# Kernel optimization log

Hardware: AMD Instinct MI355X
Metric: run time of the kernel (lower is better)

## Reference

```python
import jax, jax.numpy as jnp
import numpy as np

DIM = 1024
HEADS = 16
DIM_HEAD = 64
INNER = HEADS * DIM_HEAD
SCALE = DIM_HEAD ** -0.5


def setup_inputs() -> dict:
    key = jax.random.key(0)
    ks = jax.random.split(key, 9)
    B, N = 4, 4096
    x = jax.random.normal(ks[0], (B, N, DIM), dtype=jnp.float32)
    mask = jnp.ones((B, N), dtype=bool)
    s = 0.02
    W_qkv = jax.random.normal(ks[1], (DIM, INNER * 3), dtype=jnp.float32) * s
    w_q = jax.random.normal(ks[2], (DIM_HEAD,), dtype=jnp.float32) * s
    w_k = jax.random.normal(ks[3], (DIM_HEAD,), dtype=jnp.float32) * s
    W_r = jax.random.normal(ks[4], (DIM_HEAD, DIM_HEAD), dtype=jnp.float32) * s
    b_r = jnp.zeros((DIM_HEAD,), dtype=jnp.float32)
    W_out = jax.random.normal(ks[5], (INNER, DIM), dtype=jnp.float32) * s
    b_out = jnp.zeros((DIM,), dtype=jnp.float32)
    return {"x": x, "mask": mask, "W_qkv": W_qkv, "w_q": w_q, "w_k": w_k,
            "W_r": W_r, "b_r": b_r, "W_out": W_out, "b_out": b_out}


def reference(x, mask, W_qkv, w_q, w_k, W_r, b_r, W_out, b_out):
    B, N, D = x.shape
    h, dh = HEADS, DIM_HEAD
    mask_value = -jnp.finfo(x.dtype).max

    qkv = x @ W_qkv                                  # [B,N,3*inner]
    q, k, v = jnp.split(qkv, 3, axis=-1)
    tohead = lambda t: t.reshape(B, N, h, dh).transpose(0, 2, 1, 3)  # b h n d
    q, k, v = tohead(q), tohead(k), tohead(v)
    m = mask[:, None, :]                             # b 1 n

    # global query via softmax-pooled per-token logits
    q_logits = jnp.einsum('bhnd,d->bhn', q, w_q) * SCALE
    q_attn = jax.nn.softmax(jnp.where(m, q_logits, mask_value), axis=-1)
    global_q = jnp.einsum('bhn,bhnd->bhd', q_attn, q)[:, :, None, :]  # b h 1 d

    k = k * global_q
    k_logits = jnp.einsum('bhnd,d->bhn', k, w_k) * SCALE
    k_attn = jax.nn.softmax(jnp.where(m, k_logits, mask_value), axis=-1)
    global_k = jnp.einsum('bhn,bhnd->bhd', k_attn, k)[:, :, None, :]  # b h 1 d

    v = v * global_k
    r = jnp.einsum('bhnd,de->bhne', v, W_r) + b_r + q  # to_r(v) + q
    r = r.transpose(0, 2, 1, 3).reshape(B, N, h * dh)  # b n (h d)
    return r @ W_out + b_out
```

## Files before the change

### kernel.cpp

```cpp
#include <hip/hip_runtime.h>
#include <hip/hip_bf16.h>
#include <math.h>

#define B_    4
#define N_    4096
#define D_    1024
#define H_    16
#define DH_   64
#define M_TOT (B_ * N_)
#define QKV3  (3 * D_)
#define SCALE_ 0.125f
#define NSPLIT 8

typedef float f32x4 __attribute__((ext_vector_type(4)));
typedef __bf16 bf16x8 __attribute__((ext_vector_type(8)));
typedef unsigned short u16;
typedef unsigned int u32;

__device__ __forceinline__ float bf2f(u16 u) {
    union { u32 i; float f; } v; v.i = ((u32)u) << 16; return v.f;
}
__device__ __forceinline__ u16 f2bf(float f) {
    union { float f; u32 i; } v; v.f = f;
    u32 r = (v.i + 0x7fffu + ((v.i >> 16) & 1u)) >> 16;
    return (u16)r;
}

__global__ __launch_bounds__(256) void prep(const float* __restrict__ x, u16* __restrict__ xb,
                                            const float* __restrict__ Wqkv, u16* __restrict__ wqkv,
                                            const float* __restrict__ Wout, u16* __restrict__ wout) {
    __shared__ float t[32][33];
    const int bid = blockIdx.x, tid = threadIdx.x;
    if (bid < 16384) {
        const int i = bid * 256 + tid;
        float4 v = ((const float4*)x)[i];
        ushort4 o;
        o.x = f2bf(v.x); o.y = f2bf(v.y); o.z = f2bf(v.z); o.w = f2bf(v.w);
        ((ushort4*)xb)[i] = o;
        return;
    }
    const float* in; u16* out; int K, N, bx, by;
    if (bid < 16384 + 3072) {
        const int b2 = bid - 16384;
        in = Wqkv; out = wqkv; K = D_; N = QKV3; bx = b2 % 96; by = b2 / 96;
    } else {
        const int b2 = bid - 19456;
        in = Wout; out = wout; K = D_; N = D_; bx = b2 & 31; by = b2 >> 5;
    }
    const int n0 = bx * 32, k0 = by * 32;
    const int tx = tid & 31, ty = tid >> 5;
#pragma unroll
    for (int r = 0; r < 32; r += 8)
        t[ty + r][tx] = in[(size_t)(k0 + ty + r) * N + n0 + tx];
    __syncthreads();
#pragma unroll
    for (int r = 0; r < 32; r += 8)
        out[(size_t)(n0 + ty + r) * K + k0 + tx] = f2bf(t[tx][ty + r]);
}

#define BM 256
#define BN 256
#define BK 32

template <bool SCATTER, bool SWIZ>
__global__ __launch_bounds__(512, 2) void gemm_bt(const u16* __restrict__ A,
                                                  const u16* __restrict__ Bt,
                                                  void* __restrict__ Cout,
                                                  const float* __restrict__ bias,
                                                  int M, int N, int K) {
    __shared__ u16 lds[65536];
    const int tid = threadIdx.x;
    const int lane = tid & 63, wave = tid >> 6;
    const int wm = wave >> 2, wn = wave & 3;
    u32 bx = blockIdx.x, by = blockIdx.y;
    if (SWIZ) {
        const u32 nwg = gridDim.x * gridDim.y;
        const u32 lid = by * gridDim.x + bx;
        const u32 chunk = nwg >> 3;
        const u32 nid = (lid & 7) * chunk + (lid >> 3);
        bx = nid % gridDim.x; by = nid / gridDim.x;
    }
    const int m0 = by * BM, n0 = bx * BN;

    const int srow = tid >> 2;
    const int scol = 8 * ((tid & 3) ^ ((tid >> 3) & 3));
    const u16* aSrc = A + (size_t)(m0 + srow) * K + scol;
    const u16* bSrc = Bt + (size_t)(n0 + srow) * K + scol;
    const u32 dOff = (u32)wave * 512u;

    const int cbu = 8 * ((lane >> 4) ^ ((lane >> 1) & 3));
    const u32 arow = (u32)(wm * 128 + (lane & 15)) * 32u + cbu;
    const u32 brow = 32768u + (u32)(wn * 64 + (lane & 15)) * 32u + cbu;

    f32x4 acc[8][4] = {};

#define GLOAD(src, off) __builtin_amdgcn_global_load_lds(                          \
        (__attribute__((address_space(1))) const void*)(src),                      \
        (__attribute__((address_space(3))) void*)&lds[off], 16, 0, 0)
#define STAGE(t) { const size_t ko = (size_t)(t) * BK; const u32 sb_ = ((t) & 3) * 8192u; \
        GLOAD(aSrc + ko,                   sb_ + dOff);                            \
        GLOAD(aSrc + ko + (size_t)128 * K, sb_ + 4096u + dOff);                    \
        GLOAD(bSrc + ko,                   32768u + sb_ + dOff);                   \
        GLOAD(bSrc + ko + (size_t)128 * K, 32768u + sb_ + 4096u + dOff); }

    const int NT = K >> 5;
    STAGE(0); STAGE(1); STAGE(2);

    for (int t = 0; t < NT; ++t) {
        if (t + 3 <= NT)      asm volatile("s_waitcnt vmcnt(8)" ::: "memory");
        else if (t + 2 == NT) asm volatile("s_waitcnt vmcnt(4)" ::: "memory");
        else                  asm volatile("s_waitcnt vmcnt(0)" ::: "memory");
        __builtin_amdgcn_s_barrier();
        if (t + 3 < NT) STAGE(t + 3);

        const u32 sb = (u32)(t & 3) * 8192u;
        bf16x8 af[8], bfr[4];
#pragma unroll
        for (int i = 0; i < 8; i++) af[i] = *(const bf16x8*)&lds[sb + arow + i * 512];
#pragma unroll
        for (int j = 0; j < 4; j++) bfr[j] = *(const bf16x8*)&lds[sb + brow + j * 512];
        __builtin_amdgcn_s_setprio(1);
#pragma unroll
        for (int i = 0; i < 8; i++)
#pragma unroll
            for (int j = 0; j < 4; j++)
                acc[i][j] = __builtin_amdgcn_mfma_f32_16x16x32_bf16(af[i], bfr[j], acc[i][j], 0, 0, 0);
        __builtin_amdgcn_s_setprio(0);
    }
#undef STAGE
#undef GLOAD

    __syncthreads();
    const int cr = (lane >> 4) * 4;
    const int cc = lane & 15;
    u16* reg = &lds[(u32)wave * 8192u];

    if (SCATTER) {
#pragma unroll
        for (int i = 0; i < 8; i++)
#pragma unroll
            for (int j = 0; j < 4; j++)
#pragma unroll
                for (int r = 0; r < 4; r++)
                    reg[(i * 16 + cr + r) * 64 + j * 16 + cc] = f2bf(acc[i][j][r]);
        const int colb = n0 + wn * 64;
        const int part = colb >> 10, hh = (colb >> 6) & (H_ - 1);
        const int grow0 = m0 + wm * 128;
        const int bb = grow0 >> 12, nn0 = grow0 & (N_ - 1);
        u16* plane = (u16*)Cout + (((size_t)(part * B_ + bb) * H_ + hh) * N_) * DH_;
        const int lr8 = lane >> 3, le = (lane & 7) * 8;
#pragma unroll
        for (int p = 0; p < 16; p++) {
            const int lr = p * 8 + lr8;
            const uint4 w = *(const uint4*)&reg[lr * 64 + le];
            *(uint4*)(plane + (size_t)(nn0 + lr) * DH_ + le) = w;
        }
    } else {
        float* regf = (float*)reg;
        const int lr4 = lane >> 4, le4 = (lane & 15) * 4;
        float bv[4];
#pragma unroll
        for (int j = 0; j < 4; j++)
            bv[j] = bias ? bias[n0 + wn * 64 + j * 16 + cc] : 0.f;
#pragma unroll
        for (int h = 0; h < 2; h++) {
#pragma unroll
            for (int i2 = 0; i2 < 4; i2++) {
                const int i = h * 4 + i2;
#pragma unroll
                for (int j = 0; j < 4; j++)
#pragma unroll
                    for (int r = 0; r < 4; r++)
                        regf[(i2 * 16 + cr + r) * 64 + j * 16 + cc] = acc[i][j][r] + bv[j];
            }
#pragma unroll
            for (int p = 0; p < 16; p++) {
                const int lr = p * 4 + lr4;
                const float4 w = *(const float4*)&regf[lr * 64 + le4];
                *(float4*)((float*)Cout + (size_t)(m0 + wm * 128 + h * 64 + lr) * N
                           + n0 + wn * 64 + le4) = w;
            }
            if (!h) __syncthreads();
        }
    }
}

template <bool KPHASE>
__global__ __launch_bounds__(256) void pool_partial(const u16* __restrict__ plane,
                                                    const float* __restrict__ wvec,
                                                    const float* __restrict__ partq,
                                                    float* __restrict__ part) {
    __shared__ float sm[32], sl[32], sacc[32][64];
    __shared__ float gqsh[64];
    const int bh = blockIdx.x, s = blockIdx.y;
    const int tid = threadIdx.x;
    const int sub = tid >> 3, j = tid & 7;
    const size_t base = (size_t)bh * N_ * DH_ + (size_t)s * (N_ / NSPLIT) * DH_ + j * 8;

    if (KPHASE) {
        if (tid < 64) {
            float M = -INFINITY;
            for (int t = 0; t < NSPLIT; t++) M = fmaxf(M, partq[((size_t)bh * NSPLIT + t) * 66]);
            float L = 0.f, ssum = 0.f;
            for (int t = 0; t < NSPLIT; t++) {
                const float* o = partq + ((size_t)bh * NSPLIT + t) * 66;
                const float e = __expf(o[0] - M);
                L += o[1] * e;
                ssum += o[2 + tid] * e;
            }
            gqsh[tid] = ssum / L;
        }
        __syncthreads();
    }

    float wv[8], gq[8];
#pragma unroll
    for (int i = 0; i < 8; i++) wv[i] = wvec[j * 8 + i];
    if (KPHASE) {
#pragma unroll
        for (int i = 0; i < 8; i++) gq[i] = gqsh[j * 8 + i];
    }

    float m = -INFINITY, l = 0.f, acc[8];
#pragma unroll
    for (int i = 0; i < 8; i++) acc[i] = 0.f;
    const int ITER = N_ / NSPLIT / 32;
    uint4 raw = *(const uint4*)(plane + base + (size_t)sub * DH_);
    for (int it = 0; it < ITER; it++) {
        uint4 nxt;
        if (it + 1 < ITER)
            nxt = *(const uint4*)(plane + base + (size_t)((it + 1) * 32 + sub) * DH_);
        const u16* pu = (const u16*)&raw;
        float f[8], p = 0.f;
#pragma unroll
        for (int i = 0; i < 8; i++) {
            f[i] = bf2f(pu[i]);
            if (KPHASE) f[i] *= gq[i];
            p += f[i] * wv[i];
        }
        p += __shfl_xor(p, 1); p += __shfl_xor(p, 2); p += __shfl_xor(p, 4);
        p *= SCALE_;
        const float mn = fmaxf(m, p);
        const float sc = __expf(m - mn);
        const float w = __expf(p - mn);
        m = mn; l = l * sc + w;
#pragma unroll
        for (int i = 0; i < 8; i++) acc[i] = acc[i] * sc + w * f[i];
        raw = nxt;
    }
    if (j == 0) { sm[sub] = m; sl[sub] = l; }
#pragma unroll
    for (int i = 0; i < 8; i++) sacc[sub][j * 8 + i] = acc[i];
    __syncthreads();
    if (tid < 64) {
        float M = -INFINITY;
        for (int g = 0; g < 32; g++) M = fmaxf(M, sm[g]);
        float L = 0.f, ssum = 0.f;
        for (int g = 0; g < 32; g++) {
            const float e = __expf(sm[g] - M);
            L += sl[g] * e;
            ssum += sacc[g][tid] * e;
        }
        float* o = part + ((size_t)bh * NSPLIT + s) * 66;
        if (tid == 0) { o[0] = M; o[1] = L; }
        o[2 + tid] = ssum;
    }
}

__global__ __launch_bounds__(256) void apply_r_mfma(const u16* __restrict__ qkv,
                                                    const float* __restrict__ Wr,
                                                    const float* __restrict__ br,
                                                    const float* __restrict__ partk,
                                                    u16* __restrict__ rout) {
    __shared__ u16 Mt[64][136];
    __shared__ float gksh[64];
    __shared__ u16 rb[4][64 * 64];
    const int bh = blockIdx.y;
    const int b = bh >> 4, h = bh & 15;
    const int tid = threadIdx.x, lane = tid & 63, wave = tid >> 6;

    if (tid < 64) {
        float M = -INFINITY;
        for (int t = 0; t < NSPLIT; t++) M = fmaxf(M, partk[((size_t)bh * NSPLIT + t) * 66]);
        float L = 0.f, ssum = 0.f;
        for (int t = 0; t < NSPLIT; t++) {
            const float* o = partk + ((size_t)bh * NSPLIT + t) * 66;
            const float e = __expf(o[0] - M);
            L += o[1] * e;
            ssum += o[2 + tid] * e;
        }
        gksh[tid] = ssum / L;
    }
    __syncthreads();

    for (int idx = tid; idx < 4096; idx += 256) {
        const int d = idx >> 6, e = idx & 63;
        Mt[e][d] = f2bf(gksh[d] * Wr[idx]);
        Mt[e][64 + d] = (d == e) ? (u16)0x3F80 : (u16)0;
    }
    __syncthreads();

    const size_t qbase = (size_t)bh * N_ * DH_;
    const size_t vbase = (size_t)(2 * B_ * H_ + bh) * N_ * DH_;
    const int row0 = blockIdx.x * 256 + wave * 64;
    const int fr = lane & 15;
    const int fk8 = (lane >> 4) * 8;
    f32x4 acc[4][4] = {};

#pragma unroll
    for (int ks = 0; ks < 4; ks++) {
        const int kd = ks * 32 + fk8;
        bf16x8 af[4], bf[4];
#pragma unroll
        for (int i = 0; i < 4; i++) {
            const int row = row0 + i * 16 + fr;
            const size_t off = (kd < 64) ? (vbase + (size_t)row * DH_ + kd)
                                         : (qbase + (size_t)row * DH_ + (kd - 64));
            af[i] = *(const bf16x8*)(qkv + off);
        }
#pragma unroll
        for (int j = 0; j < 4; j++)
            bf[j] = *(const bf16x8*)&Mt[j * 16 + fr][kd];
#pragma unroll
        for (int i = 0; i < 4; i++)
#pragma unroll
            for (int j = 0; j < 4; j++)
                acc[i][j] = __builtin_amdgcn_mfma_f32_16x16x32_bf16(af[i], bf[j], acc[i][j], 0, 0, 0);
    }

    const int cr = (lane >> 4) * 4;
    const int cc = lane & 15;
#pragma unroll
    for (int j = 0; j < 4; j++) {
        const float bv = br[j * 16 + cc];
#pragma unroll
        for (int i = 0; i < 4; i++)
#pragma unroll
            for (int r = 0; r < 4; r++)
                rb[wave][(i * 16 + cr + r) * 64 + j * 16 + cc] = f2bf(acc[i][j][r] + bv);
    }
    const int lr8 = lane >> 3, le = (lane & 7) * 8;
#pragma unroll
    for (int p = 0; p < 8; p++) {
        const int lr = p * 8 + lr8;
        const uint4 w = *(const uint4*)&rb[wave][lr * 64 + le];
        *(uint4*)(rout + (size_t)(b * N_ + row0 + lr) * D_ + h * DH_ + le) = w;
    }
}

extern "C" void kernel_launch(void* const* d_in, const int* in_sizes, int n_in,
                              void* d_out, int out_size, void* d_ws, size_t ws_size,
                              hipStream_t stream) {
    const float* x = (const float*)d_in[0];
    const float* W_qkv = (const float*)d_in[2];
    const float* w_q = (const float*)d_in[3];
    const float* w_k = (const float*)d_in[4];
    const float* W_r = (const float*)d_in[5];
    const float* b_r = (const float*)d_in[6];
    const float* W_out = (const float*)d_in[7];
    const float* b_out = (const float*)d_in[8];
    float* out = (float*)d_out;

    u16* xb = (u16*)d_ws;
    u16* wqkv = xb + (size_t)M_TOT * D_;
    u16* wout = wqkv + (size_t)QKV3 * D_;
    u16* qkv = wout + (size_t)D_ * D_;
    u16* rbuf = qkv + (size_t)M_TOT * QKV3;
    float* partq = (float*)(rbuf + (size_t)M_TOT * D_);
    float* partk = partq + 64 * NSPLIT * 66;

    prep<<<16384 + 3072 + 1024, 256, 0, stream>>>(x, xb, W_qkv, wqkv, W_out, wout);

    gemm_bt<true, true><<<dim3(QKV3 / BN, M_TOT / BM), 512, 0, stream>>>(
        xb, wqkv, qkv, nullptr, M_TOT, QKV3, D_);

    pool_partial<false><<<dim3(64, NSPLIT), 256, 0, stream>>>(qkv, w_q, nullptr, partq);
    pool_partial<true><<<dim3(64, NSPLIT), 256, 0, stream>>>(
        qkv + (size_t)(B_ * H_) * N_ * DH_, w_k, partq, partk);

    apply_r_mfma<<<dim3(N_ / 256, 64), 256, 0, stream>>>(qkv, W_r, b_r, partk, rbuf);

    gemm_bt<false, false><<<dim3(D_ / BN, M_TOT / BM), 512, 0, stream>>>(
        rbuf, wout, out, b_out, M_TOT, D_, D_);
}
```

Baseline: 330.1 us.

## Split GEMM main loop into two barrier-separated half-tile MFMA phases

Each K-step of the bf16 GEMM mainloop is split into two halves. The first computes rows 0-3 of the A fragments while the A-tile prefetch for step t+3 is issued. The second loads rows 4-7, issues the B-tile prefetch and waits, then runs the remaining MFMAs. Explicit lgkmcnt waits and sched_barriers fix the order of LDS reads against MFMA issue. The aim is better overlap of global-to-LDS traffic and LDS reads with matrix-core work across waves. It costs extra workgroup barriers per iteration and depends on exact vmcnt accounting. The output-projection GEMM's second template flag is also switched to true, which turns on an alternate code path for that launch.

New measurement: 334.5 us. About the same (+1.3%).

```diff
diff --git a/kernel.cpp b/kernel.cpp
--- a/kernel.cpp
+++ b/kernel.cpp
@@ -97,37 +97,57 @@
 #define GLOAD(src, off) __builtin_amdgcn_global_load_lds(                          \
         (__attribute__((address_space(1))) const void*)(src),                      \
         (__attribute__((address_space(3))) void*)&lds[off], 16, 0, 0)
-#define STAGE(t) { const size_t ko = (size_t)(t) * BK; const u32 sb_ = ((t) & 3) * 8192u; \
+#define SA(t) { const size_t ko = (size_t)(t) * BK; const u32 sb_ = ((t) & 3) * 8192u; \
         GLOAD(aSrc + ko,                   sb_ + dOff);                            \
-        GLOAD(aSrc + ko + (size_t)128 * K, sb_ + 4096u + dOff);                    \
+        GLOAD(aSrc + ko + (size_t)128 * K, sb_ + 4096u + dOff); }
+#define SB(t) { const size_t ko = (size_t)(t) * BK; const u32 sb_ = ((t) & 3) * 8192u; \
         GLOAD(bSrc + ko,                   32768u + sb_ + dOff);                   \
         GLOAD(bSrc + ko + (size_t)128 * K, 32768u + sb_ + 4096u + dOff); }
 
     const int NT = K >> 5;
-    STAGE(0); STAGE(1); STAGE(2);
+    SA(0); SB(0); SA(1); SB(1); SA(2); SB(2);
+    asm volatile("s_waitcnt vmcnt(8)" ::: "memory");
+    __builtin_amdgcn_s_barrier();
 
     for (int t = 0; t < NT; ++t) {
-        if (t + 3 <= NT)      asm volatile("s_waitcnt vmcnt(8)" ::: "memory");
-        else if (t + 2 == NT) asm volatile("s_waitcnt vmcnt(4)" ::: "memory");
-        else                  asm volatile("s_waitcnt vmcnt(0)" ::: "memory");
+        const u32 sb = (u32)(t & 3) * 8192u;
+        bf16x8 afA[4], bfr[4], afB[4];
+#pragma unroll
+        for (int i = 0; i < 4; i++) afA[i] = *(const bf16x8*)&lds[sb + arow + i * 512];
+#pragma unroll
+        for (int j = 0; j < 4; j++) bfr[j] = *(const bf16x8*)&lds[sb + brow + j * 512];
+        if (t + 3 < NT) SA(t + 3);
         __builtin_amdgcn_s_barrier();
-        if (t + 3 < NT) STAGE(t + 3);
-
-        const u32 sb = (u32)(t & 3) * 8192u;
-        bf16x8 af[8], bfr[4];
-#pragma unroll
-        for (int i = 0; i < 8; i++) af[i] = *(const bf16x8*)&lds[sb + arow + i * 512];
-#pragma unroll
-        for (int j = 0; j < 4; j++) bfr[j] = *(const bf16x8*)&lds[sb + brow + j * 512];
+        asm volatile("s_waitcnt lgkmcnt(0)" ::: "memory");
+        __builtin_amdgcn_sched_barrier(0);
         __builtin_amdgcn_s_setprio(1);
 #pragma unroll
-        for (int i = 0; i < 8; i++)
+        for (int i = 0; i < 4; i++)
 #pragma unroll
             for (int j = 0; j < 4; j++)
-                acc[i][j] = __builtin_amdgcn_mfma_f32_16x16x32_bf16(af[i], bfr[j], acc[i][j], 0, 0, 0);
+                acc[i][j] = __builtin_amdgcn_mfma_f32_16x16x32_bf16(afA[i], bfr[j], acc[i][j], 0, 0, 0);
         __builtin_amdgcn_s_setprio(0);
-    }
-#undef STAGE
+        __builtin_amdgcn_s_barrier();
+#pragma unroll
+        for (int i = 0; i < 4; i++) afB[i] = *(const bf16x8*)&lds[sb + arow + (4 + i) * 512];
+        if (t + 3 < NT) SB(t + 3);
+        if (t + 3 < NT)      asm volatile("s_waitcnt vmcnt(8)" ::: "memory");
+        else if (t + 2 < NT) asm volatile("s_waitcnt vmcnt(4)" ::: "memory");
+        else if (t + 1 < NT) asm volatile("s_waitcnt vmcnt(0)" ::: "memory");
+        __builtin_amdgcn_s_barrier();
+        asm volatile("s_waitcnt lgkmcnt(0)" ::: "memory");
+        __builtin_amdgcn_sched_barrier(0);
+        __builtin_amdgcn_s_setprio(1);
+#pragma unroll
+        for (int i = 0; i < 4; i++)
+#pragma unroll
+            for (int j = 0; j < 4; j++)
+                acc[4 + i][j] = __builtin_amdgcn_mfma_f32_16x16x32_bf16(afB[i], bfr[j], acc[4 + i][j], 0, 0, 0);
+        __builtin_amdgcn_s_setprio(0);
+        __builtin_amdgcn_s_barrier();
+    }
+#undef SA
+#undef SB
 #undef GLOAD
 
     __syncthreads();
@@ -380,6 +400,6 @@
 
     apply_r_mfma<<<dim3(N_ / 256, 64), 256, 0, stream>>>(qkv, W_r, b_r, partk, rbuf);
 
-    gemm_bt<false, false><<<dim3(D_ / BN, M_TOT / BM), 512, 0, stream>>>(
+    gemm_bt<false, true><<<dim3(D_ / BN, M_TOT / BM), 512, 0, stream>>>(
         rbuf, wout, out, b_out, M_TOT, D_, D_);
 }
```

## Fuse query softmax pooling into QKV GEMM epilogue and drop q-pool kernel

Applied to the files above, without the earlier changes.

The QKV GEMM epilogue now computes the per-token q logits and an online-softmax partial (max, sum, weighted q) for each 128-row wave tile, using fp32 accumulators. This removes the separate pool_partial pass over the q plane. pool_k merges 32 partials instead of 8. The prep kernel now converts 8 float4 per thread, and the output GEMM switches on the grid swizzle. The fused path adds shuffles and exps to the GEMM epilogue for one third of its tiles, which can add register pressure.

New measurement: 328.1 us. About the same (-0.6%).

```diff
diff --git a/kernel.cpp b/kernel.cpp
--- a/kernel.cpp
+++ b/kernel.cpp
@@ -11,6 +11,7 @@
 #define QKV3  (3 * D_)
 #define SCALE_ 0.125f
 #define NSPLIT 8
+#define NSQ    32
 
 typedef float f32x4 __attribute__((ext_vector_type(4)));
 typedef __bf16 bf16x8 __attribute__((ext_vector_type(8)));
@@ -31,20 +32,24 @@
                                             const float* __restrict__ Wout, u16* __restrict__ wout) {
     __shared__ float t[32][33];
     const int bid = blockIdx.x, tid = threadIdx.x;
-    if (bid < 16384) {
-        const int i = bid * 256 + tid;
-        float4 v = ((const float4*)x)[i];
-        ushort4 o;
-        o.x = f2bf(v.x); o.y = f2bf(v.y); o.z = f2bf(v.z); o.w = f2bf(v.w);
-        ((ushort4*)xb)[i] = o;
+    if (bid < 2048) {
+        const int base = bid * 2048 + tid;
+#pragma unroll
+        for (int k = 0; k < 8; k++) {
+            const int i = base + k * 256;
+            float4 v = ((const float4*)x)[i];
+            ushort4 o;
+            o.x = f2bf(v.x); o.y = f2bf(v.y); o.z = f2bf(v.z); o.w = f2bf(v.w);
+            ((ushort4*)xb)[i] = o;
+        }
         return;
     }
     const float* in; u16* out; int K, N, bx, by;
-    if (bid < 16384 + 3072) {
-        const int b2 = bid - 16384;
+    if (bid < 2048 + 3072) {
+        const int b2 = bid - 2048;
         in = Wqkv; out = wqkv; K = D_; N = QKV3; bx = b2 % 96; by = b2 / 96;
     } else {
-        const int b2 = bid - 19456;
+        const int b2 = bid - 5120;
         in = Wout; out = wout; K = D_; N = D_; bx = b2 & 31; by = b2 >> 5;
     }
     const int n0 = bx * 32, k0 = by * 32;
@@ -62,11 +67,13 @@
 #define BN 256
 #define BK 32
 
-template <bool SCATTER, bool SWIZ>
+template <bool SCATTER, bool SWIZ, bool QPOOL>
 __global__ __launch_bounds__(512, 2) void gemm_bt(const u16* __restrict__ A,
                                                   const u16* __restrict__ Bt,
                                                   void* __restrict__ Cout,
                                                   const float* __restrict__ bias,
+                                                  const float* __restrict__ wqv,
+                                                  float* __restrict__ partq,
                                                   int M, int N, int K) {
     __shared__ u16 lds[65536];
     const int tid = threadIdx.x;
@@ -136,17 +143,60 @@
     u16* reg = &lds[(u32)wave * 8192u];
 
     if (SCATTER) {
-#pragma unroll
-        for (int i = 0; i < 8; i++)
-#pragma unroll
-            for (int j = 0; j < 4; j++)
-#pragma unroll
-                for (int r = 0; r < 4; r++)
-                    reg[(i * 16 + cr + r) * 64 + j * 16 + cc] = f2bf(acc[i][j][r]);
         const int colb = n0 + wn * 64;
         const int part = colb >> 10, hh = (colb >> 6) & (H_ - 1);
         const int grow0 = m0 + wm * 128;
         const int bb = grow0 >> 12, nn0 = grow0 & (N_ - 1);
+
+        if (QPOOL && part == 0) {
+            float wq4[4];
+#pragma unroll
+            for (int j = 0; j < 4; j++) wq4[j] = wqv[j * 16 + cc];
+            float m = -INFINITY, l = 0.f, s4[4] = {0.f, 0.f, 0.f, 0.f};
+#pragma unroll
+            for (int i = 0; i < 8; i++)
+#pragma unroll
+                for (int r = 0; r < 4; r++) {
+                    float p = acc[i][0][r] * wq4[0] + acc[i][1][r] * wq4[1]
+                            + acc[i][2][r] * wq4[2] + acc[i][3][r] * wq4[3];
+                    p += __shfl_xor(p, 1); p += __shfl_xor(p, 2);
+                    p += __shfl_xor(p, 4); p += __shfl_xor(p, 8);
+                    p *= SCALE_;
+                    const float mn = fmaxf(m, p);
+                    const float e = __expf(m - mn), w = __expf(p - mn);
+                    l = l * e + w;
+#pragma unroll
+                    for (int j = 0; j < 4; j++) s4[j] = s4[j] * e + w * acc[i][j][r];
+                    m = mn;
+                }
+#pragma unroll
+            for (int d = 16; d <= 32; d <<= 1) {
+                const float m2 = __shfl_xor(m, d), l2 = __shfl_xor(l, d);
+                float s42[4];
+#pragma unroll
+                for (int j = 0; j < 4; j++) s42[j] = __shfl_xor(s4[j], d);
+                const float M2 = fmaxf(m, m2);
+                const float e1 = __expf(m - M2), e2 = __expf(m2 - M2);
+                l = l * e1 + l2 * e2;
+#pragma unroll
+                for (int j = 0; j < 4; j++) s4[j] = s4[j] * e1 + s42[j] * e2;
+                m = M2;
+            }
+            float* o = partq + ((size_t)(bb * H_ + hh) * NSQ + (nn0 >> 7)) * 66;
+            if (lane < 16) {
+#pragma unroll
+                for (int j = 0; j < 4; j++) o[2 + j * 16 + lane] = s4[j];
+                if (lane == 0) { o[0] = m; o[1] = l; }
+            }
+        }
+
+#pragma unroll
+        for (int i = 0; i < 8; i++)
+#pragma unroll
+            for (int j = 0; j < 4; j++)
+#pragma unroll
+                for (int r = 0; r < 4; r++)
+                    reg[(i * 16 + cr + r) * 64 + j * 16 + cc] = f2bf(acc[i][j][r]);
         u16* plane = (u16*)Cout + (((size_t)(part * B_ + bb) * H_ + hh) * N_) * DH_;
         const int lr8 = lane >> 3, le = (lane & 7) * 8;
 #pragma unroll
@@ -185,11 +235,10 @@
     }
 }
 
-template <bool KPHASE>
-__global__ __launch_bounds__(256) void pool_partial(const u16* __restrict__ plane,
-                                                    const float* __restrict__ wvec,
-                                                    const float* __restrict__ partq,
-                                                    float* __restrict__ part) {
+__global__ __launch_bounds__(256) void pool_k(const u16* __restrict__ plane,
+                                              const float* __restrict__ wvec,
+                                              const float* __restrict__ partq,
+                                              float* __restrict__ part) {
     __shared__ float sm[32], sl[32], sacc[32][64];
     __shared__ float gqsh[64];
     const int bh = blockIdx.x, s = blockIdx.y;
@@ -197,29 +246,23 @@
     const int sub = tid >> 3, j = tid & 7;
     const size_t base = (size_t)bh * N_ * DH_ + (size_t)s * (N_ / NSPLIT) * DH_ + j * 8;
 
-    if (KPHASE) {
-        if (tid < 64) {
-            float M = -INFINITY;
-            for (int t = 0; t < NSPLIT; t++) M = fmaxf(M, partq[((size_t)bh * NSPLIT + t) * 66]);
-            float L = 0.f, ssum = 0.f;
-            for (int t = 0; t < NSPLIT; t++) {
-                const float* o = partq + ((size_t)bh * NSPLIT + t) * 66;
-                const float e = __expf(o[0] - M);
-                L += o[1] * e;
-                ssum += o[2 + tid] * e;
-            }
-            gqsh[tid] = ssum / L;
-        }
-        __syncthreads();
-    }
+    if (tid < 64) {
+        float M = -INFINITY;
+        for (int t = 0; t < NSQ; t++) M = fmaxf(M, partq[((size_t)bh * NSQ + t) * 66]);
+        float L = 0.f, ssum = 0.f;
+        for (int t = 0; t < NSQ; t++) {
+            const float* o = partq + ((size_t)bh * NSQ + t) * 66;
+            const float e = __expf(o[0] - M);
+            L += o[1] * e;
+            ssum += o[2 + tid] * e;
+        }
+        gqsh[tid] = ssum / L;
+    }
+    __syncthreads();
 
     float wv[8], gq[8];
 #pragma unroll
-    for (int i = 0; i < 8; i++) wv[i] = wvec[j * 8 + i];
-    if (KPHASE) {
-#pragma unroll
-        for (int i = 0; i < 8; i++) gq[i] = gqsh[j * 8 + i];
-    }
+    for (int i = 0; i < 8; i++) { wv[i] = wvec[j * 8 + i]; gq[i] = gqsh[j * 8 + i]; }
 
     float m = -INFINITY, l = 0.f, acc[8];
 #pragma unroll
@@ -234,8 +277,7 @@
         float f[8], p = 0.f;
 #pragma unroll
         for (int i = 0; i < 8; i++) {
-            f[i] = bf2f(pu[i]);
-            if (KPHASE) f[i] *= gq[i];
+            f[i] = bf2f(pu[i]) * gq[i];
             p += f[i] * wv[i];
         }
         p += __shfl_xor(p, 1); p += __shfl_xor(p, 2); p += __shfl_xor(p, 4);
@@ -367,19 +409,18 @@
     u16* qkv = wout + (size_t)D_ * D_;
     u16* rbuf = qkv + (size_t)M_TOT * QKV3;
     float* partq = (float*)(rbuf + (size_t)M_TOT * D_);
-    float* partk = partq + 64 * NSPLIT * 66;
-
-    prep<<<16384 + 3072 + 1024, 256, 0, stream>>>(x, xb, W_qkv, wqkv, W_out, wout);
-
-    gemm_bt<true, true><<<dim3(QKV3 / BN, M_TOT / BM), 512, 0, stream>>>(
-        xb, wqkv, qkv, nullptr, M_TOT, QKV3, D_);
-
-    pool_partial<false><<<dim3(64, NSPLIT), 256, 0, stream>>>(qkv, w_q, nullptr, partq);
-    pool_partial<true><<<dim3(64, NSPLIT), 256, 0, stream>>>(
+    float* partk = partq + 64 * NSQ * 66;
+
+    prep<<<6144, 256, 0, stream>>>(x, xb, W_qkv, wqkv, W_out, wout);
+
+    gemm_bt<true, true, true><<<dim3(QKV3 / BN, M_TOT / BM), 512, 0, stream>>>(
+        xb, wqkv, qkv, nullptr, w_q, partq, M_TOT, QKV3, D_);
+
+    pool_k<<<dim3(64, NSPLIT), 256, 0, stream>>>(
         qkv + (size_t)(B_ * H_) * N_ * DH_, w_k, partq, partk);
 
     apply_r_mfma<<<dim3(N_ / 256, 64), 256, 0, stream>>>(qkv, W_r, b_r, partk, rbuf);
 
-    gemm_bt<false, false><<<dim3(D_ / BN, M_TOT / BM), 512, 0, stream>>>(
-        rbuf, wout, out, b_out, M_TOT, D_, D_);
-}
+    gemm_bt<false, true, false><<<dim3(D_ / BN, M_TOT / BM), 512, 0, stream>>>(
+        rbuf, wout, out, b_out, nullptr, nullptr, M_TOT, D_, D_);
+}
```
